# Performance work log

Hardware: AMD Instinct MI355X
Metric: run time of the kernel (lower is better)

Reference implementation:

```python
import jax, jax.numpy as jnp
import numpy as np

MAX_DISP = 4                 # max_displacement
OUT_DIM = 2 * MAX_DISP + 1   # 9 -> 81 displacement channels


def setup_inputs() -> dict:
    key = jax.random.key(0)
    k1, k2 = jax.random.split(key)
    B, C, H, W = 8, 64, 192, 192
    x1 = jax.random.normal(k1, (B, C, H, W), dtype=jnp.float32)
    x2 = jax.random.normal(k2, (B, C, H, W), dtype=jnp.float32)
    return {"x1": x1, "x2": x2}


def reference(x1, x2):
    # x1, x2: [B, C, H, W]; stride1 = stride2 = 1 (default-equivalent config)
    B, C, H, W = x1.shape
    # pad x2 by max_displacement on each spatial side
    x2p = jnp.pad(x2, ((0, 0), (0, 0), (MAX_DISP, MAX_DISP), (MAX_DISP, MAX_DISP)))
    # for each displacement (i, j): channel-mean of x1 * shifted window of x2
    cv = [
        jnp.mean(x1 * jax.lax.dynamic_slice(x2p, (0, 0, i, j), (B, C, H, W)), axis=1)
        for i in range(OUT_DIM)
        for j in range(OUT_DIM)
    ]
    # torch.cat of keepdim means == stack along channel: [B, OUT_DIM**2, H, W]
    return jnp.stack(cv, axis=1)
```

## Files before the change

kernel.cpp:

```cpp
#include <hip/hip_runtime.h>


constexpr int MAXD = 4;
constexpr int OD   = 9;
constexpr int ND   = 81;
constexpr int TB_W = 32;
constexpr int TB_H = 16;
constexpr int TWp  = 8;
constexpr int NT   = 256;

constexpr int Bc = 8, Cc = 64, Hc = 192, Wc = 192;
constexpr int HW = Hc * Wc;
constexpr int GX = Wc / TB_W;
constexpr int GY = Hc / TB_H;
constexpr int NTILE = GX * GY;
constexpr int UPI   = NTILE * OD;
constexpr int NBLK  = Bc * UPI / 4;

__global__ __launch_bounds__(NT, 2) void corr_kernel(
    const float* __restrict__ x1, const float* __restrict__ x2,
    float* __restrict__ out)
{
    const int tid  = threadIdx.x;
    const int lane = tid & 63;
    const int wid  = tid >> 6;
    const int px8  = (lane & 3) * 8;
    const int gh   = lane >> 2;

    const int B    = blockIdx.x;
    const int b    = B & 7;
    const int up   = (B >> 3) * 4 + wid;
    const int di   = up % OD;
    const int tile = up / OD;
    const int ty   = tile / GX;
    const int tx   = tile - ty * GX;
    const int w0   = tx * TB_W;
    const int h0   = ty * TB_H;

    const float* x1b = x1 + (long)b * Cc * HW;
    const float* x2b = x2 + (long)b * Cc * HW;

    const int r1 = h0 + gh;
    const int cb = w0 + px8;
    const int rg = r1 + di - MAXD;
    const bool rowok = (unsigned)rg < (unsigned)Hc;
    const int rgc = min(max(rg, 0), Hc - 1);
    const int cc0 = (cb >= 4) ? (cb - 4) : 0;
    const int cc3 = (cb <= Wc - 12) ? (cb + 8) : (Wc - 4);

    const int o1 = r1  * Wc + cb;
    const int e0 = rgc * Wc + cc0;
    const int e1 = rgc * Wc + cb;
    const int e3 = rgc * Wc + cc3;

    float acc[OD][TWp];
#pragma unroll
    for (int dj = 0; dj < OD; ++dj)
#pragma unroll
        for (int p = 0; p < TWp; ++p) acc[dj][p] = 0.f;

#pragma unroll 4
    for (int c = 0; c < Cc; ++c) {
        const float* p1 = x1b + c * HW;
        const float* p2 = x2b + c * HW;
        float4 a0 = *(const float4*)(p1 + o1);
        float4 a1 = *(const float4*)(p1 + o1 + 4);
        float4 q0 = *(const float4*)(p2 + e0);
        float4 q1 = *(const float4*)(p2 + e1);
        float4 q2 = *(const float4*)(p2 + e1 + 4);
        float4 q3 = *(const float4*)(p2 + e3);
        float wn[16] = {q0.x,q0.y,q0.z,q0.w,  q1.x,q1.y,q1.z,q1.w,
                        q2.x,q2.y,q2.z,q2.w,  q3.x,q3.y,q3.z,q3.w};
        float av[8]  = {a0.x,a0.y,a0.z,a0.w,  a1.x,a1.y,a1.z,a1.w};
#pragma unroll
        for (int dj = 0; dj < OD; ++dj)
#pragma unroll
            for (int p = 0; p < TWp; ++p)
                acc[dj][p] = fmaf(av[p], wn[p + dj], acc[dj][p]);
    }

    const float sc = 1.0f / 64.0f;
    float* ob = out + (((long)b * ND + di * OD) * Hc + r1) * Wc + cb;
#pragma unroll
    for (int dj = 0; dj < OD; ++dj) {
        float v[TWp];
#pragma unroll
        for (int p = 0; p < TWp; ++p) {
            const bool ok = rowok && ((unsigned)(cb + p + dj - MAXD) < (unsigned)Wc);
            v[p] = ok ? acc[dj][p] * sc : 0.f;
        }
        float4 v0 = {v[0], v[1], v[2], v[3]};
        float4 v1 = {v[4], v[5], v[6], v[7]};
        *(float4*)(ob + (long)dj * HW)     = v0;
        *(float4*)(ob + (long)dj * HW + 4) = v1;
    }
}

extern "C" void kernel_launch(void* const* d_in, const int* in_sizes, int n_in,
                              void* d_out, int out_size, void* d_ws, size_t ws_size,
                              hipStream_t stream) {
    const float* x1 = (const float*)d_in[0];
    const float* x2 = (const float*)d_in[1];
    float* out = (float*)d_out;
    corr_kernel<<<dim3(NBLK), NT, 0, stream>>>(x1, x2, out);
}
```

Measured before the change: 340.6 us.

## Triple-buffer channel loads with explicit register banks and pointer increments

Restructures the channel loop into a three-stage register pipeline: the loads for upcoming channels are issued while FMAs run on the current bank, to hide global memory latency. Addressing switches to pointers that are incremented by one plane per channel. The launch-bounds occupancy hint is replaced by amdgpu_waves_per_eu(2,3). The extra live float4 banks raise register pressure, which may reduce occupancy or cause spills.

```diff
diff --git a/kernel.cpp b/kernel.cpp
--- a/kernel.cpp
+++ b/kernel.cpp
@@ -17,9 +17,12 @@
 constexpr int UPI   = NTILE * OD;
 constexpr int NBLK  = Bc * UPI / 4;
 
-__global__ __launch_bounds__(NT, 2) void corr_kernel(
-    const float* __restrict__ x1, const float* __restrict__ x2,
-    float* __restrict__ out)
+struct Bank { float4 a0, a1, q0, q1, q2, q3; };
+
+__global__ __launch_bounds__(NT)
+__attribute__((amdgpu_waves_per_eu(2, 3)))
+void corr_kernel(const float* __restrict__ x1, const float* __restrict__ x2,
+                 float* __restrict__ out)
 {
     const int tid  = threadIdx.x;
     const int lane = tid & 63;
@@ -48,10 +51,10 @@
     const int cc0 = (cb >= 4) ? (cb - 4) : 0;
     const int cc3 = (cb <= Wc - 12) ? (cb + 8) : (Wc - 4);
 
-    const int o1 = r1  * Wc + cb;
-    const int e0 = rgc * Wc + cc0;
-    const int e1 = rgc * Wc + cb;
-    const int e3 = rgc * Wc + cc3;
+    const float* pa  = x1b + (r1  * Wc + cb);
+    const float* pb0 = x2b + (rgc * Wc + cc0);
+    const float* pb1 = x2b + (rgc * Wc + cb);
+    const float* pb3 = x2b + (rgc * Wc + cc3);
 
     float acc[OD][TWp];
 #pragma unroll
@@ -59,25 +62,42 @@
 #pragma unroll
         for (int p = 0; p < TWp; ++p) acc[dj][p] = 0.f;
 
-#pragma unroll 4
-    for (int c = 0; c < Cc; ++c) {
-        const float* p1 = x1b + c * HW;
-        const float* p2 = x2b + c * HW;
-        float4 a0 = *(const float4*)(p1 + o1);
-        float4 a1 = *(const float4*)(p1 + o1 + 4);
-        float4 q0 = *(const float4*)(p2 + e0);
-        float4 q1 = *(const float4*)(p2 + e1);
-        float4 q2 = *(const float4*)(p2 + e1 + 4);
-        float4 q3 = *(const float4*)(p2 + e3);
-        float wn[16] = {q0.x,q0.y,q0.z,q0.w,  q1.x,q1.y,q1.z,q1.w,
-                        q2.x,q2.y,q2.z,q2.w,  q3.x,q3.y,q3.z,q3.w};
-        float av[8]  = {a0.x,a0.y,a0.z,a0.w,  a1.x,a1.y,a1.z,a1.w};
+    auto LOAD = [&](Bank& bk) {
+        bk.a0 = *(const float4*)(pa);
+        bk.a1 = *(const float4*)(pa + 4);
+        bk.q0 = *(const float4*)(pb0);
+        bk.q1 = *(const float4*)(pb1);
+        bk.q2 = *(const float4*)(pb1 + 4);
+        bk.q3 = *(const float4*)(pb3);
+        pa += HW; pb0 += HW; pb1 += HW; pb3 += HW;
+    };
+
+    auto FMA = [&](const Bank& bk) {
+        float wn[16] = {bk.q0.x, bk.q0.y, bk.q0.z, bk.q0.w,
+                        bk.q1.x, bk.q1.y, bk.q1.z, bk.q1.w,
+                        bk.q2.x, bk.q2.y, bk.q2.z, bk.q2.w,
+                        bk.q3.x, bk.q3.y, bk.q3.z, bk.q3.w};
+        float av[8]  = {bk.a0.x, bk.a0.y, bk.a0.z, bk.a0.w,
+                        bk.a1.x, bk.a1.y, bk.a1.z, bk.a1.w};
 #pragma unroll
         for (int dj = 0; dj < OD; ++dj)
 #pragma unroll
             for (int p = 0; p < TWp; ++p)
                 acc[dj][p] = fmaf(av[p], wn[p + dj], acc[dj][p]);
+    };
+
+    Bank A, Bb, Cb;
+    LOAD(A); LOAD(Bb); LOAD(Cb);
+#pragma unroll 1
+    for (int t = 0; t < 20; ++t) {
+        FMA(A);  LOAD(A);
+        FMA(Bb); LOAD(Bb);
+        FMA(Cb); LOAD(Cb);
     }
+    FMA(A); LOAD(A);
+    FMA(Bb);
+    FMA(Cb);
+    FMA(A);
 
     const float sc = 1.0f / 64.0f;
     float* ob = out + (((long)b * ND + di * OD) * Hc + r1) * Wc + cb;
```

Result: no change. 335.9 us (-1.4%).
